# Kernel optimization log

Measured on AMD Instinct MI355X. Metric: run time of the kernel, lower is better.

## Reference

```python
import jax, jax.numpy as jnp
import numpy as np

E = 65536      # num edges
T = 262144     # num triplets
H = 128        # hidden_channels
D = 64         # int_emb_size
C = 8          # basis_emb_size
NR = 6         # num_radial
NS = 7         # num_spherical
NB = 6         # len(bt_list) = num_BT + 1
BT_LIST = (-1, 0, 1, 2, 3, 4)
NBS = 1        # num_before_skip (also used for after-skip list in original code)


def setup_inputs() -> dict:
    key = jax.random.key(0)
    ks = iter(jax.random.split(key, 40))
    s = 0.05
    p = lambda shape: jax.random.normal(next(ks), shape, dtype=jnp.float32) * s
    inp = dict(
        x=jax.random.normal(next(ks), (E, H), dtype=jnp.float32),
        rbf=jax.random.normal(next(ks), (E, NR), dtype=jnp.float32),
        sbf=jax.random.normal(next(ks), (T, NS * NR), dtype=jnp.float32),
        idx_kj=jax.random.randint(next(ks), (T,), 0, E),
        idx_ji=jax.random.randint(next(ks), (T,), 0, E),
        bt=jax.random.randint(next(ks), (E,), 0, 5),
        lambda_d=1,
        alpha=jnp.float32(0.7),
        # per-branch stacked weights (6 branches)
        W_kj=p((NB, H, H)), b_kj=jnp.zeros((NB, H), jnp.float32),
        W_rbf1=p((NB, NR, C)), W_rbf2=p((NB, C, H)),
        W_sbf1=p((NB, NS * NR, C)), W_sbf2=p((NB, C, D)),
        W_down=p((NB, H, D)),
        W_ji=p((H, H)), b_ji=jnp.zeros((H,), jnp.float32),
        W_up=p((D, H)),
        rb1_w=p((NBS, H, H)), rb1_b=jnp.zeros((NBS, H), jnp.float32),
        rb2_w=p((NBS, H, H)), rb2_b=jnp.zeros((NBS, H), jnp.float32),
        W_lin=p((H, H)), b_lin=jnp.zeros((H,), jnp.float32),
        ra1_w=p((NBS, H, H)), ra1_b=jnp.zeros((NBS, H), jnp.float32),
        ra2_w=p((NBS, H, H)), ra2_b=jnp.zeros((NBS, H), jnp.float32),
    )
    return inp


def reference(x, rbf, sbf, idx_kj, idx_ji, bt, lambda_d, alpha,
              W_kj, b_kj, W_rbf1, W_rbf2, W_sbf1, W_sbf2, W_down,
              W_ji, b_ji, W_up, rb1_w, rb1_b, rb2_w, rb2_b,
              W_lin, b_lin, ra1_w, ra1_b, ra2_w, ra2_b):
    act = jax.nn.silu

    x_ji = act(x @ W_ji + b_ji)                                  # [E,H]

    # per-branch edge transforms, vectorized over the 6 branches (axis b)
    tmp = act(jnp.einsum('eh,bhg->beg', x, W_kj) + b_kj[:, None, :])   # [B,E,H]
    rbf_p = jnp.einsum('er,brc->bec', rbf, W_rbf1)                     # [B,E,C]
    rbf_p = jnp.einsum('bec,bcg->beg', rbf_p, W_rbf2)                  # [B,E,H]
    tmp = tmp * rbf_p
    down = act(jnp.einsum('beh,bhd->bed', tmp, W_down))                # [B,E,D]

    sbf_p = jnp.einsum('ts,bsc->btc', sbf, W_sbf1)                     # [B,T,C]
    sbf_p = jnp.einsum('btc,bcd->btd', sbf_p, W_sbf2)                  # [B,T,D]

    spe = down[:, idx_kj, :] * sbf_p                                   # [B,T,D]

    # last branch scattered with weight alpha
    x_kj_tot = alpha * jax.ops.segment_sum(spe[-1], idx_ji, num_segments=E)

    # per band-type masked scatter with weight (1 - alpha)
    bt_trip = bt[idx_kj]                                               # [T]
    for b, btv in enumerate(BT_LIST):
        m = (bt_trip == btv).astype(x.dtype)[:, None]
        x_kj_tot = x_kj_tot + (1.0 - alpha) * jax.ops.segment_sum(
            spe[b] * m, idx_ji, num_segments=E)

    x_kj = act(x_kj_tot @ W_up)                                        # [E,H]
    h = x_ji + x_kj
    for i in range(rb1_w.shape[0]):
        h = h + act(act(h @ rb1_w[i] + rb1_b[i]) @ rb2_w[i] + rb2_b[i])
    h = act(h @ W_lin + b_lin) + x
    for i in range(ra1_w.shape[0]):
        h = h + act(act(h @ ra1_w[i] + ra1_b[i]) @ ra2_w[i] + ra2_b[i])
    return h
```

## Files before the change

kernel.cpp:

```cpp
#include <hip/hip_runtime.h>
#include <hip/hip_bf16.h>
#include <stdint.h>

typedef __bf16 bf16_t;
typedef bf16_t bf16x8 __attribute__((ext_vector_type(8)));
typedef bf16_t bf16x2 __attribute__((ext_vector_type(2)));
typedef float f32x4 __attribute__((ext_vector_type(4)));

#define E_N 65536
#define T_N 262144
#define CAP 16
#define OVF_MAX T_N

__device__ __forceinline__ float silu_f(float v) {
  return v / (1.0f + __expf(-v));
}

__device__ __forceinline__ int permrow(int n) {
  return (n & ~31) | ((n & 1) << 4) | ((n & 30) >> 1);
}

__device__ __forceinline__ uint32_t pack_bf16(float a, float b) {
  union { bf16x2 h; uint32_t u; } u;
  u.h[0] = (bf16_t)a; u.h[1] = (bf16_t)b;
  return u.u;
}

__device__ __forceinline__ void g2l16(const void* g, void* l) {
  __builtin_amdgcn_global_load_lds(
      (const __attribute__((address_space(1))) void*)g,
      (__attribute__((address_space(3))) void*)l, 16, 0, 0);
}

template<int KI, int NTJ>
__device__ __forceinline__ void gemm_tile(const bf16_t* A, const bf16_t* B,
                                          int mb, int nb, int l16, int q,
                                          f32x4 (&acc)[2][NTJ]) {
#pragma unroll
  for (int kt = 0; kt < KI; ++kt) {
    const int sw = ((kt * 4 + q) ^ l16) << 3;
    bf16x8 a0 = *(const bf16x8*)(A + ((mb + l16) << 7) + sw);
    bf16x8 a1 = *(const bf16x8*)(A + ((mb + 16 + l16) << 7) + sw);
#pragma unroll
    for (int tj = 0; tj < NTJ; ++tj) {
      bf16x8 b = *(const bf16x8*)(B + ((nb + tj * 16 + l16) << 7) + sw);
      acc[0][tj] = __builtin_amdgcn_mfma_f32_16x16x32_bf16(a0, b, acc[0][tj], 0, 0, 0);
      acc[1][tj] = __builtin_amdgcn_mfma_f32_16x16x32_bf16(a1, b, acc[1][tj], 0, 0, 0);
    }
  }
}

template<int C4>
__device__ __forceinline__ void stage_x(bf16_t* dst, const float* src, int tid) {
  const float4* g = (const float4*)src;
#pragma unroll
  for (int i = tid; i < 64 * C4; i += 256) {
    const int row = i / C4, c4 = i % C4;
    float4 v = g[i];
    bf16_t t[4] = {(bf16_t)v.x, (bf16_t)v.y, (bf16_t)v.z, (bf16_t)v.w};
    *(uint2*)(dst + (row << 7) + ((((c4 >> 1) ^ (row & 15)) << 3) | ((c4 & 1) << 2))) =
        *(const uint2*)t;
  }
}

__global__ __launch_bounds__(256, 4)
void prep_c8_kernel(
    const float* __restrict__ W_ji, const float* __restrict__ W_kj,
    const float* __restrict__ W_down, const float* __restrict__ W_up,
    const float* __restrict__ rb1, const float* __restrict__ rb2,
    const float* __restrict__ W_lin, const float* __restrict__ ra1,
    const float* __restrict__ ra2, const float* __restrict__ W_rbf1,
    const float* __restrict__ W_rbf2, const float* __restrict__ x,
    char* __restrict__ wm_img, char* __restrict__ wdn_img,
    char* __restrict__ pset, bf16_t* __restrict__ wcb,
    bf16_t* __restrict__ ximg,
    const float* __restrict__ sbf, const int* __restrict__ idx_kj,
    const int* __restrict__ idx_ji, const int* __restrict__ bt,
    const float* __restrict__ Wsbf1,
    float* __restrict__ c8g, uint32_t* __restrict__ meta,
    int* __restrict__ cnt, int* __restrict__ list,
    int* __restrict__ ovf)
{
  __shared__ __align__(16) union {
    bf16_t tile[64 * 128];
    struct {
      float s_sbf[64 * 44];
      float s_W1[2016];
      float s_c8[64 * 16];
      int s_bs[64];
    } c;
  } S;

  const int tid = threadIdx.x;
  const int blk = blockIdx.x;

  if (blk < 4096) {
    const int base = blk * 64;

    for (int i = tid; i < 2016; i += 256) S.c.s_W1[i] = Wsbf1[i];
    if (tid < 64) {
      const int t = base + tid;
      const int kj = idx_kj[t];
      const int ji = idx_ji[t];
      const int bs = bt[kj] + 1;
      S.c.s_bs[tid] = bs;
      meta[t] = (uint32_t)kj | ((uint32_t)bs << 16);
      const int pos = atomicAdd(&cnt[ji], 1);
      if (pos < CAP) {
        list[ji * CAP + pos] = t;
      } else {
        const int o = atomicAdd(&ovf[0], 1);
        if (o < OVF_MAX) { ovf[2 + 2 * o] = t; ovf[2 + 2 * o + 1] = ji; }
      }
    }
    {
      const float2* sg = (const float2*)(sbf + (size_t)base * 42);
      for (int i = tid; i < 64 * 21; i += 256) {
        const int r = i / 21, c2 = i - r * 21;
        const float2 v = sg[i];
        S.c.s_sbf[r * 44 + c2 * 2] = v.x;
        S.c.s_sbf[r * 44 + c2 * 2 + 1] = v.y;
      }
    }
    __syncthreads();

    {
      const int i = tid >> 2;
      const int brr = (tid >> 1) & 1;
      const int cg = tid & 1;
      const int b = brr ? S.c.s_bs[i] : 5;
      const float* w = &S.c.s_W1[b * 336 + cg * 4];
      const float* sb = &S.c.s_sbf[i * 44];
      float a0 = 0.f, a1 = 0.f, a2 = 0.f, a3 = 0.f;
#pragma unroll
      for (int s = 0; s < 42; ++s) {
        const float sv = sb[s];
        const float* ws = w + s * 8;
        a0 += sv * ws[0]; a1 += sv * ws[1]; a2 += sv * ws[2]; a3 += sv * ws[3];
      }
      float* dc = &S.c.s_c8[i * 16 + brr * 8 + cg * 4];
      dc[0] = a0; dc[1] = a1; dc[2] = a2; dc[3] = a3;
    }
    __syncthreads();

    {
      const float4* s4 = (const float4*)S.c.s_c8;
      float4* g4 = (float4*)(c8g + (size_t)base * 16);
      g4[tid] = s4[tid];
    }
    return;
  }

  const int pblk = blk - 4096;
  if (pblk >= 115) {
    const int t = pblk - 115;
    stage_x<32>(S.tile, x + (size_t)t * 8192, tid);
    __syncthreads();
    uint4* dst = (uint4*)(ximg + (size_t)t * 8192);
    const uint4* s = (const uint4*)S.tile;
#pragma unroll
    for (int i = 0; i < 4; ++i) dst[i * 256 + tid] = s[i * 256 + tid];
    return;
  }
  if (pblk >= 112) {
    const int o = (pblk - 112) * 256 + tid;
    if (o < 640) {
      const int b = o >> 7, n = o & 127;
      bf16_t t[8];
#pragma unroll
      for (int r = 0; r < 6; ++r) {
        const float* w1 = W_rbf1 + (b + 1) * 48 + r * 8;
        const float* w2 = W_rbf2 + (b + 1) * 1024 + n;
        float s = 0.f;
#pragma unroll
        for (int c = 0; c < 8; ++c) s += w1[c] * w2[c * 128];
        t[r] = (bf16_t)s;
      }
      t[6] = (bf16_t)0.f; t[7] = (bf16_t)0.f;
      *(uint4*)(wcb + (b * 128 + n) * 8) = *(const uint4*)t;
    }
    return;
  }
  if (pblk >= 108) {
    const int item = (pblk - 108) * 256 + tid;
    const int n = item >> 3, k8 = item & 7;
    bf16_t t[8];
#pragma unroll
    for (int j = 0; j < 8; ++j) t[j] = (bf16_t)W_up[(k8 * 8 + j) * 128 + n];
    const int row = permrow(n);
    *(uint4*)((bf16_t*)pset + (row << 7) + ((k8 ^ (row & 15)) << 3)) = *(const uint4*)t;
    return;
  }
  if (pblk >= 88) {
    const int item = (pblk - 88) * 256 + tid;
    const int m = item >> 10, w = item & 1023;
    const int n = w >> 4, k8 = w & 15;
    const float* src = W_down + (m + 1) * 8192;
    bf16_t* img = (bf16_t*)(wdn_img + m * 16384);
    bf16_t t[8];
#pragma unroll
    for (int j = 0; j < 8; ++j) t[j] = (bf16_t)src[(k8 * 8 + j) * 64 + n];
    const int row = permrow(n);
    *(uint4*)(img + (row << 7) + ((k8 ^ (row & 15)) << 3)) = *(const uint4*)t;
    return;
  }
  const int item = pblk * 256 + tid;
  const int m = item >> 11, w = item & 2047;
  const int n = w >> 4, k8 = w & 15;
  const float* src; char* img;
  if (m == 0)      { src = W_ji;             img = wm_img; }
  else if (m <= 5) { src = W_kj + m * 16384; img = wm_img + m * 32768; }
  else if (m == 6) { src = rb1;   img = pset + 1 * 32768; }
  else if (m == 7) { src = rb2;   img = pset + 2 * 32768; }
  else if (m == 8) { src = W_lin; img = pset + 3 * 32768; }
  else if (m == 9) { src = ra1;   img = pset + 4 * 32768; }
  else             { src = ra2;   img = pset + 5 * 32768; }
  bf16_t t[8];
#pragma unroll
  for (int j = 0; j < 8; ++j) t[j] = (bf16_t)src[(k8 * 8 + j) * 128 + n];
  const int row = permrow(n);
  *(uint4*)((bf16_t*)img + (row << 7) + ((k8 ^ (row & 15)) << 3)) = *(const uint4*)t;
}

__global__ __launch_bounds__(256, 3)
void edge_kernel(const bf16_t* __restrict__ ximg, const float* __restrict__ rbf,
                 const float* __restrict__ b_kj, const float* __restrict__ b_ji,
                 const char* __restrict__ wm_img, const char* __restrict__ wdn_img,
                 const bf16_t* __restrict__ wcb,
                 bf16_t* __restrict__ x_ji_out, bf16_t* __restrict__ down)
{
  __shared__ __align__(16) bf16_t xA[64 * 128];
  __shared__ __align__(16) bf16_t Wb[128 * 128];
  __shared__ __align__(16) bf16_t wcbS[128 * 8];
  __shared__ __align__(16) bf16_t rbfS[64 * 8];
  __shared__ float biasS[128];

  const int tid = threadIdx.x;
  const int lane = tid & 63, wv = tid >> 6;
  const int q = lane >> 4, l16 = lane & 15;
  const int mb = (wv >> 1) * 32, nb = (wv & 1) * 64;
  const int eb = blockIdx.x;
  const int br = eb % 6;
  const int tile = eb / 6;
  const int R = tile * 64;

  {
    const char* xs = (const char*)(ximg + (size_t)tile * 8192);
    char* xd = (char*)xA;
#pragma unroll
    for (int c = 0; c < 4; ++c) {
      const int off = (c * 4 + wv) * 1024 + lane * 16;
      g2l16(xs + off, xd + off);
    }
    const char* wsrc = wm_img + (size_t)br * 32768;
    char* wd = (char*)Wb;
#pragma unroll
    for (int c = 0; c < 8; ++c) {
      const int off = (c * 4 + wv) * 1024 + lane * 16;
      g2l16(wsrc + off, wd + off);
    }
  }
  if (br == 0) {
    if (tid < 128) biasS[tid] = b_ji[tid];
  } else {
    if (tid < 128) biasS[tid] = b_kj[br * 128 + tid];
    if (wv < 2) {
      const char* cs = (const char*)(wcb + (size_t)(br - 1) * 1024);
      const int off = wv * 1024 + lane * 16;
      g2l16(cs + off, (char*)wcbS + off);
    }
    if (tid < 64) {
      const float* rg = rbf + (size_t)(R + tid) * 6;
      bf16_t t[8] = {(bf16_t)rg[0], (bf16_t)rg[1], (bf16_t)rg[2],
                     (bf16_t)rg[3], (bf16_t)rg[4], (bf16_t)rg[5],
                     (bf16_t)0.f, (bf16_t)0.f};
      *(uint4*)(rbfS + tid * 8) = *(const uint4*)t;
    }
  }
  __syncthreads();

  f32x4 acc[2][4] = {};
  gemm_tile<4, 4>(xA, Wb, mb, nb, l16, q, acc);

  if (br == 0) {
#pragma unroll
    for (int ti = 0; ti < 2; ++ti)
#pragma unroll
      for (int r = 0; r < 4; ++r) {
        const int row = mb + ti * 16 + q * 4 + r;
#pragma unroll
        for (int gl = 0; gl < 2; ++gl) {
          const int col0 = nb + gl * 32 + 2 * l16;
          const float2 b2 = *(const float2*)&biasS[col0];
          *(uint32_t*)&x_ji_out[(size_t)(R + row) * 128 + col0] =
              pack_bf16(silu_f(acc[ti][2 * gl][r] + b2.x),
                        silu_f(acc[ti][2 * gl + 1][r] + b2.y));
        }
      }
    return;
  }

  __syncthreads();

  {
    const char* ds = wdn_img + (size_t)(br - 1) * 16384;
    char* dd = (char*)Wb;
#pragma unroll
    for (int c = 0; c < 4; ++c) {
      const int off = (c * 4 + wv) * 1024 + lane * 16;
      g2l16(ds + off, dd + off);
    }
  }

  float wc[2][2][6];
#pragma unroll
  for (int gl = 0; gl < 2; ++gl)
#pragma unroll
    for (int j = 0; j < 2; ++j) {
      const int col = nb + gl * 32 + 2 * l16 + j;
      bf16x8 w8 = *(const bf16x8*)&wcbS[col * 8];
#pragma unroll
      for (int c = 0; c < 6; ++c) wc[gl][j][c] = (float)w8[c];
    }
#pragma unroll
  for (int ti = 0; ti < 2; ++ti)
#pragma unroll
    for (int r = 0; r < 4; ++r) {
      const int row = mb + ti * 16 + q * 4 + r;
      bf16x8 rv8 = *(const bf16x8*)&rbfS[row * 8];
      float rv[6];
#pragma unroll
      for (int c = 0; c < 6; ++c) rv[c] = (float)rv8[c];
#pragma unroll
      for (int gl = 0; gl < 2; ++gl) {
        const int col0 = nb + gl * 32 + 2 * l16;
        const float2 b2 = *(const float2*)&biasS[col0];
        float p0 = 0.f, p1 = 0.f;
#pragma unroll
        for (int c = 0; c < 6; ++c) {
          p0 += rv[c] * wc[gl][0][c];
          p1 += rv[c] * wc[gl][1][c];
        }
        const float v0 = silu_f(acc[ti][2 * gl][r] + b2.x) * p0;
        const float v1 = silu_f(acc[ti][2 * gl + 1][r] + b2.y) * p1;
        *(uint32_t*)&xA[(row << 7) + ((((col0 >> 3) ^ (row & 15)) << 3) | (col0 & 7))] =
            pack_bf16(v0, v1);
      }
    }
  __syncthreads();

  const int nb2 = (wv & 1) * 32;
  f32x4 acc2[2][2] = {};
  gemm_tile<4, 2>(xA, Wb, mb, nb2, l16, q, acc2);
#pragma unroll
  for (int ti = 0; ti < 2; ++ti)
#pragma unroll
    for (int r = 0; r < 4; ++r) {
      const int row = mb + ti * 16 + q * 4 + r;
      const int col0 = nb2 + 2 * l16;
      *(uint32_t*)&down[((size_t)(br - 1) * E_N + R + row) * 64 + col0] =
          pack_bf16(silu_f(acc2[ti][0][r]), silu_f(acc2[ti][1][r]));
    }
}

__global__ __launch_bounds__(256, 8)
void gather_kernel(const int* __restrict__ cnt, const int* __restrict__ list,
                   const uint32_t* __restrict__ meta, const float* __restrict__ c8g,
                   const float* __restrict__ Wsbf2, const bf16_t* __restrict__ down,
                   const float* __restrict__ alpha_p, const int* __restrict__ ovf,
                   float* __restrict__ xkj)
{
  __shared__ float sW2[3072];
  for (int i = threadIdx.x; i < 3072; i += 256) sW2[i] = Wsbf2[i];
  __syncthreads();

  const int e = blockIdx.x * 4 + (threadIdx.x >> 6);
  const int j = threadIdx.x & 63;
  const float alpha = alpha_p[0], oma = 1.f - alpha;
  const float* w5 = &sW2[5 * 512 + j];

  int n = cnt[e];
  if (n > CAP) n = CAP;

  int tk = 0; uint32_t mk = 0;
  if ((j & 15) < n) {
    tk = list[e * CAP + (j & 15)];
    mk = meta[tk];
  }

  float acc = 0.f;
  const int nn = (n + 1) & ~1;
  for (int k0 = 0; k0 < nn; k0 += 2) {
    const int k1 = (k0 + 1 < n) ? k0 + 1 : n - 1;
    const float sc1 = (k0 + 1 < n) ? 1.f : 0.f;
    const int t0 = __builtin_amdgcn_readfirstlane(__shfl(tk, k0, 64));
    const uint32_t m0 = __builtin_amdgcn_readfirstlane(__shfl(mk, k0, 64));
    const int t1 = __builtin_amdgcn_readfirstlane(__shfl(tk, k1, 64));
    const uint32_t m1 = __builtin_amdgcn_readfirstlane(__shfl(mk, k1, 64));
    const int kj0 = m0 & 0xffff, b0 = m0 >> 16;
    const int kj1 = m1 & 0xffff, b1 = m1 >> 16;
    const float g5a = (float)down[((size_t)4 * E_N + kj0) * 64 + j];
    const float gba = (float)down[((size_t)(b0 - 1) * E_N + kj0) * 64 + j];
    const float g5b = (float)down[((size_t)4 * E_N + kj1) * 64 + j];
    const float gbb = (float)down[((size_t)(b1 - 1) * E_N + kj1) * 64 + j];
    const float* cp0 = c8g + (size_t)t0 * 16;
    const float* cp1 = c8g + (size_t)t1 * 16;
    float d5a = 0.f, dba = 0.f, d5b = 0.f, dbb = 0.f;
#pragma unroll
    for (int c = 0; c < 8; ++c) {
      d5a += cp0[c]     * w5[c * 64];
      dba += cp0[8 + c] * sW2[b0 * 512 + c * 64 + j];
      d5b += cp1[c]     * w5[c * 64];
      dbb += cp1[8 + c] * sW2[b1 * 512 + c * 64 + j];
    }
    acc += alpha * g5a * d5a + oma * gba * dba;
    acc += sc1 * (alpha * g5b * d5b + oma * gbb * dbb);
  }

  const int oc = ovf[0];
  for (int k = 0; k < oc; ++k) {
    const int ji = ovf[2 + 2 * k + 1];
    if (ji != e) continue;
    const int t = ovf[2 + 2 * k];
    const uint32_t m = meta[t];
    const int kj = m & 0xffff;
    const int b  = m >> 16;
    const float g5 = (float)down[((size_t)4 * E_N + kj) * 64 + j];
    const float gb = (float)down[((size_t)(b - 1) * E_N + kj) * 64 + j];
    const float* cp = c8g + (size_t)t * 16;
    float d5 = 0.f, db = 0.f;
#pragma unroll
    for (int c = 0; c < 8; ++c) {
      d5 += cp[c]     * w5[c * 64];
      db += cp[8 + c] * sW2[b * 512 + c * 64 + j];
    }
    acc += alpha * g5 * d5 + oma * gb * db;
  }

  xkj[(size_t)e * 64 + j] = acc;
}

__global__ __launch_bounds__(256, 3)
void epi_kernel(const float* __restrict__ x, const bf16_t* __restrict__ x_ji,
                const float* __restrict__ xkj, const char* __restrict__ pset,
                const float* __restrict__ rb1_b, const float* __restrict__ rb2_b,
                const float* __restrict__ lin_b, const float* __restrict__ ra1_b,
                const float* __restrict__ ra2_b,
                float* __restrict__ out)
{
  __shared__ __align__(16) bf16_t buf[64 * 128];
  __shared__ __align__(16) bf16_t Wb[128 * 128];
  __shared__ float biasS[2][128];

  const int tid = threadIdx.x;
  const int lane = tid & 63, wv = tid >> 6;
  const int q = lane >> 4, l16 = lane & 15;
  const int mb = (wv >> 1) * 32, nb = (wv & 1) * 64;
  const int R = blockIdx.x * 64;

#define DMA_W(SLOT) do {                                                         \
    const char* ps_ = pset + (size_t)(SLOT) * 32768;                             \
    char* wd_ = (char*)Wb;                                                       \
    _Pragma("unroll")                                                            \
    for (int c_ = 0; c_ < 8; ++c_) {                                             \
      const int off_ = (c_ * 4 + wv) * 1024 + lane * 16;                         \
      g2l16(ps_ + off_, wd_ + off_);                                             \
    }                                                                            \
  } while (0)

  stage_x<16>(buf, xkj + (size_t)R * 64, tid);
  DMA_W(0);
  __syncthreads();

  f32x4 hreg[2][4];
  {
    f32x4 acc[2][4] = {};
    gemm_tile<2, 4>(buf, Wb, mb, nb, l16, q, acc);
    __syncthreads();
#pragma unroll
    for (int ti = 0; ti < 2; ++ti)
#pragma unroll
      for (int r = 0; r < 4; ++r) {
        const int row = mb + ti * 16 + q * 4 + r;
#pragma unroll
        for (int gl = 0; gl < 2; ++gl) {
          const int col0 = nb + gl * 32 + 2 * l16;
          union { uint32_t u; bf16x2 h; } xj;
          xj.u = *(const uint32_t*)&x_ji[(size_t)(R + row) * 128 + col0];
          const float h0 = (float)xj.h[0] + silu_f(acc[ti][2 * gl][r]);
          const float h1 = (float)xj.h[1] + silu_f(acc[ti][2 * gl + 1][r]);
          hreg[ti][2 * gl][r] = h0;
          hreg[ti][2 * gl + 1][r] = h1;
          *(uint32_t*)&buf[(row << 7) + ((((col0 >> 3) ^ (row & 15)) << 3) | (col0 & 7))] =
              pack_bf16(h0, h1);
        }
      }
    DMA_W(1);
    if (tid < 128) biasS[0][tid] = rb1_b[tid];
    __syncthreads();
  }

#define EPI_STAGE(K, NEXTSLOT, NEXTBIAS, BODY)                                   \
  {                                                                              \
    f32x4 acc[2][4] = {};                                                        \
    gemm_tile<4, 4>(buf, Wb, mb, nb, l16, q, acc);                               \
    __syncthreads();                                                             \
    const float* bs_ = biasS[((K) - 1) & 1];                                     \
    _Pragma("unroll")                                                            \
    for (int ti = 0; ti < 2; ++ti)                                               \
      _Pragma("unroll")                                                          \
      for (int r = 0; r < 4; ++r) {                                              \
        const int row = mb + ti * 16 + q * 4 + r;                                \
        _Pragma("unroll")                                                        \
        for (int gl = 0; gl < 2; ++gl) {                                         \
          const int col0 = nb + gl * 32 + 2 * l16;                               \
          const float2 b2 = *(const float2*)&bs_[col0];                          \
          const float g0 = acc[ti][2 * gl][r] + b2.x;                            \
          const float g1 = acc[ti][2 * gl + 1][r] + b2.y;                        \
          BODY                                                                   \
        }                                                                        \
      }                                                                          \
    if ((K) < 5) {                                                               \
      DMA_W(NEXTSLOT);                                                           \
      if (tid < 128) biasS[(K) & 1][tid] = NEXTBIAS[tid];                        \
      __syncthreads();                                                           \
    }                                                                            \
  }

  EPI_STAGE(1, 2, rb2_b, {
    *(uint32_t*)&buf[(row << 7) + ((((col0 >> 3) ^ (row & 15)) << 3) | (col0 & 7))] =
        pack_bf16(silu_f(g0), silu_f(g1));
  })

  EPI_STAGE(2, 3, lin_b, {
    const float h0 = hreg[ti][2 * gl][r] + silu_f(g0);
    const float h1 = hreg[ti][2 * gl + 1][r] + silu_f(g1);
    hreg[ti][2 * gl][r] = h0; hreg[ti][2 * gl + 1][r] = h1;
    *(uint32_t*)&buf[(row << 7) + ((((col0 >> 3) ^ (row & 15)) << 3) | (col0 & 7))] =
        pack_bf16(h0, h1);
  })

  EPI_STAGE(3, 4, ra1_b, {
    const float2 xv = *(const float2*)&x[(size_t)(R + row) * 128 + col0];
    const float h0 = silu_f(g0) + xv.x;
    const float h1 = silu_f(g1) + xv.y;
    hreg[ti][2 * gl][r] = h0; hreg[ti][2 * gl + 1][r] = h1;
    *(uint32_t*)&buf[(row << 7) + ((((col0 >> 3) ^ (row & 15)) << 3) | (col0 & 7))] =
        pack_bf16(h0, h1);
  })

  EPI_STAGE(4, 5, ra2_b, {
    *(uint32_t*)&buf[(row << 7) + ((((col0 >> 3) ^ (row & 15)) << 3) | (col0 & 7))] =
        pack_bf16(silu_f(g0), silu_f(g1));
  })

  EPI_STAGE(5, 0, ra2_b, {
    float2 o;
    o.x = hreg[ti][2 * gl][r] + silu_f(g0);
    o.y = hreg[ti][2 * gl + 1][r] + silu_f(g1);
    *(float2*)&out[(size_t)(R + row) * 128 + col0] = o;
  })
#undef EPI_STAGE
#undef DMA_W
}

extern "C" void kernel_launch(void* const* d_in, const int* in_sizes, int n_in,
                              void* d_out, int out_size, void* d_ws, size_t ws_size,
                              hipStream_t stream)
{
  (void)in_sizes; (void)n_in; (void)out_size; (void)ws_size;
  const float* x      = (const float*)d_in[0];
  const float* rbf    = (const float*)d_in[1];
  const float* sbf    = (const float*)d_in[2];
  const int*   idx_kj = (const int*)d_in[3];
  const int*   idx_ji = (const int*)d_in[4];
  const int*   bt     = (const int*)d_in[5];
  const float* alpha  = (const float*)d_in[7];
  const float* W_kj   = (const float*)d_in[8];
  const float* b_kj   = (const float*)d_in[9];
  const float* W_rbf1 = (const float*)d_in[10];
  const float* W_rbf2 = (const float*)d_in[11];
  const float* W_sbf1 = (const float*)d_in[12];
  const float* W_sbf2 = (const float*)d_in[13];
  const float* W_down = (const float*)d_in[14];
  const float* W_ji   = (const float*)d_in[15];
  const float* b_ji   = (const float*)d_in[16];
  const float* W_up   = (const float*)d_in[17];
  const float* rb1_w  = (const float*)d_in[18];
  const float* rb1_b  = (const float*)d_in[19];
  const float* rb2_w  = (const float*)d_in[20];
  const float* rb2_b  = (const float*)d_in[21];
  const float* W_lin  = (const float*)d_in[22];
  const float* b_lin  = (const float*)d_in[23];
  const float* ra1_w  = (const float*)d_in[24];
  const float* ra1_b  = (const float*)d_in[25];
  const float* ra2_w  = (const float*)d_in[26];
  const float* ra2_b  = (const float*)d_in[27];

  char* ws = (char*)d_ws;
  bf16_t* down   = (bf16_t*)(ws);
  bf16_t* x_ji   = (bf16_t*)(ws + 41943040);
  bf16_t* ximg   = (bf16_t*)(ws + 58720256);
  float*  xkj    = (float*) (ws + 58720256);
  char*   wm_img = ws + 75497472;
  char*   wdn_img= ws + 75694080;
  char*   pset   = ws + 75776000;
  bf16_t* wcb    = (bf16_t*)(ws + 75972608);
  float*    c8g  = (float*)   (ws + 75982848);
  uint32_t* meta = (uint32_t*)(ws + 92760064);
  int*      list = (int*)     (ws + 93808640);
  int*      cnt  = (int*)     (ws + 98002944);
  int*      ovf  = (int*)     (ws + 98265088);

  hipMemsetAsync(cnt, 0, 262144 + 8, stream);
  prep_c8_kernel<<<5235, 256, 0, stream>>>(W_ji, W_kj, W_down, W_up, rb1_w,
                                           rb2_w, W_lin, ra1_w, ra2_w, W_rbf1,
                                           W_rbf2, x, wm_img, wdn_img, pset,
                                           wcb, ximg, sbf, idx_kj, idx_ji, bt,
                                           W_sbf1, c8g, meta, cnt, list, ovf);
  edge_kernel<<<E_N / 64 * 6, 256, 0, stream>>>(ximg, rbf, b_kj, b_ji, wm_img,
                                                wdn_img, wcb, x_ji, down);
  gather_kernel<<<E_N / 4, 256, 0, stream>>>(cnt, list, meta, c8g, W_sbf2,
                                             down, alpha, ovf, xkj);
  epi_kernel<<<E_N / 64, 256, 0, stream>>>(x, x_ji, xkj, pset,
                                           rb1_b, rb2_b, b_lin, ra1_b, ra2_b,
                                           (float*)d_out);
}
```

Before: 349.8 us.

## Compute band-type branch transforms only for edges of matching band type

Edges are bucketed by band type in the prep kernel using atomic counters, and the edge kernel now computes each branch 1-4 transform only for that branch's bucket of gathered edge rows, writing a single compact down_bt array. Branches 0 (x_ji) and 5 (last branch) are still computed for all edges. This removes the computation and storage of down values that are masked out later, cutting the band-type GEMM work and the down buffer size. In exchange it adds gathered row loads and indirect stores, plus blocks that exit early, and it relies on each edge's down value being read only through its own band type.

```diff
diff --git a/kernel.cpp b/kernel.cpp
--- a/kernel.cpp
+++ b/kernel.cpp
@@ -11,6 +11,7 @@
 #define T_N 262144
 #define CAP 16
 #define OVF_MAX T_N
+#define EINV 0x7fffffff
 
 __device__ __forceinline__ float silu_f(float v) {
   return v / (1.0f + __expf(-v));
@@ -79,7 +80,7 @@
     const float* __restrict__ Wsbf1,
     float* __restrict__ c8g, uint32_t* __restrict__ meta,
     int* __restrict__ cnt, int* __restrict__ list,
-    int* __restrict__ ovf)
+    int* __restrict__ ovf, int* __restrict__ btlist, int* __restrict__ bcnt)
 {
   __shared__ __align__(16) union {
     bf16_t tile[64 * 128];
@@ -150,6 +151,15 @@
     }
     return;
   }
+  if (blk >= 5235) {
+    const int e = (blk - 5235) * 256 + tid;
+    const int bte = bt[e];
+    if (bte < 4) {
+      const int pos = atomicAdd(&bcnt[bte], 1);
+      btlist[bte * E_N + pos] = e;
+    }
+    return;
+  }
 
   const int pblk = blk - 4096;
   if (pblk >= 115) {
@@ -227,7 +237,9 @@
                  const float* __restrict__ b_kj, const float* __restrict__ b_ji,
                  const char* __restrict__ wm_img, const char* __restrict__ wdn_img,
                  const bf16_t* __restrict__ wcb,
-                 bf16_t* __restrict__ x_ji_out, bf16_t* __restrict__ down)
+                 const int* __restrict__ btlist, const int* __restrict__ bcnt,
+                 bf16_t* __restrict__ x_ji_out, bf16_t* __restrict__ down5,
+                 bf16_t* __restrict__ down_bt)
 {
   __shared__ __align__(16) bf16_t xA[64 * 128];
   __shared__ __align__(16) bf16_t Wb[128 * 128];
@@ -239,19 +251,43 @@
   const int lane = tid & 63, wv = tid >> 6;
   const int q = lane >> 4, l16 = lane & 15;
   const int mb = (wv >> 1) * 32, nb = (wv & 1) * 64;
-  const int eb = blockIdx.x;
-  const int br = eb % 6;
-  const int tile = eb / 6;
-  const int R = tile * 64;
-
-  {
-    const char* xs = (const char*)(ximg + (size_t)tile * 8192);
+  const int bid = blockIdx.x;
+
+  int br, R = 0, bkt = 0, cbase = 0, valid = 0;
+  bool bucket = false;
+  if (bid < 1024)      { br = 0; R = bid * 64; }
+  else if (bid < 2048) { br = 5; R = (bid - 1024) * 64; }
+  else {
+    bkt = (bid - 2048) >> 10;
+    cbase = ((bid - 2048) & 1023) * 64;
+    valid = bcnt[bkt];
+    if (cbase >= valid) return;
+    br = bkt + 1;
+    bucket = true;
+  }
+  const int* elist = btlist + bkt * E_N;
+
+  if (!bucket) {
+    const char* xs = (const char*)(ximg + (size_t)(R >> 6) * 8192);
     char* xd = (char*)xA;
 #pragma unroll
     for (int c = 0; c < 4; ++c) {
       const int off = (c * 4 + wv) * 1024 + lane * 16;
       g2l16(xs + off, xd + off);
     }
+  } else {
+    for (int i = tid; i < 1024; i += 256) {
+      const int lr = i >> 4, c = i & 15;
+      const int gidx = cbase + lr;
+      if (gidx < valid) {
+        const int e = elist[gidx];
+        const uint4 v = *(const uint4*)(ximg + ((size_t)(e >> 6) << 13) +
+                                        ((e & 63) << 7) + ((c ^ (e & 15)) << 3));
+        *(uint4*)(xA + (lr << 7) + ((c ^ (lr & 15)) << 3)) = v;
+      }
+    }
+  }
+  {
     const char* wsrc = wm_img + (size_t)br * 32768;
     char* wd = (char*)Wb;
 #pragma unroll
@@ -270,11 +306,16 @@
       g2l16(cs + off, (char*)wcbS + off);
     }
     if (tid < 64) {
-      const float* rg = rbf + (size_t)(R + tid) * 6;
-      bf16_t t[8] = {(bf16_t)rg[0], (bf16_t)rg[1], (bf16_t)rg[2],
-                     (bf16_t)rg[3], (bf16_t)rg[4], (bf16_t)rg[5],
-                     (bf16_t)0.f, (bf16_t)0.f};
-      *(uint4*)(rbfS + tid * 8) = *(const uint4*)t;
+      int e = EINV;
+      if (!bucket) e = R + tid;
+      else if (cbase + tid < valid) e = elist[cbase + tid];
+      if (e != EINV) {
+        const float* rg = rbf + (size_t)e * 6;
+        bf16_t t[8] = {(bf16_t)rg[0], (bf16_t)rg[1], (bf16_t)rg[2],
+                       (bf16_t)rg[3], (bf16_t)rg[4], (bf16_t)rg[5],
+                       (bf16_t)0.f, (bf16_t)0.f};
+        *(uint4*)(rbfS + tid * 8) = *(const uint4*)t;
+      }
     }
   }
   __syncthreads();
@@ -352,13 +393,20 @@
   const int nb2 = (wv & 1) * 32;
   f32x4 acc2[2][2] = {};
   gemm_tile<4, 2>(xA, Wb, mb, nb2, l16, q, acc2);
+  bf16_t* outp = bucket ? down_bt : down5;
 #pragma unroll
   for (int ti = 0; ti < 2; ++ti)
 #pragma unroll
     for (int r = 0; r < 4; ++r) {
       const int row = mb + ti * 16 + q * 4 + r;
+      int e;
+      if (!bucket) e = R + row;
+      else {
+        if (cbase + row >= valid) continue;
+        e = elist[cbase + row];
+      }
       const int col0 = nb2 + 2 * l16;
-      *(uint32_t*)&down[((size_t)(br - 1) * E_N + R + row) * 64 + col0] =
+      *(uint32_t*)&outp[(size_t)e * 64 + col0] =
           pack_bf16(silu_f(acc2[ti][0][r]), silu_f(acc2[ti][1][r]));
     }
 }
@@ -366,7 +414,8 @@
 __global__ __launch_bounds__(256, 8)
 void gather_kernel(const int* __restrict__ cnt, const int* __restrict__ list,
                    const uint32_t* __restrict__ meta, const float* __restrict__ c8g,
-                   const float* __restrict__ Wsbf2, const bf16_t* __restrict__ down,
+                   const float* __restrict__ Wsbf2, const bf16_t* __restrict__ down5,
+                   const bf16_t* __restrict__ down_bt,
                    const float* __restrict__ alpha_p, const int* __restrict__ ovf,
                    float* __restrict__ xkj)
 {
@@ -399,10 +448,12 @@
     const uint32_t m1 = __builtin_amdgcn_readfirstlane(__shfl(mk, k1, 64));
     const int kj0 = m0 & 0xffff, b0 = m0 >> 16;
     const int kj1 = m1 & 0xffff, b1 = m1 >> 16;
-    const float g5a = (float)down[((size_t)4 * E_N + kj0) * 64 + j];
-    const float gba = (float)down[((size_t)(b0 - 1) * E_N + kj0) * 64 + j];
-    const float g5b = (float)down[((size_t)4 * E_N + kj1) * 64 + j];
-    const float gbb = (float)down[((size_t)(b1 - 1) * E_N + kj1) * 64 + j];
+    const bf16_t* pb0 = (b0 == 5) ? down5 : down_bt;
+    const bf16_t* pb1 = (b1 == 5) ? down5 : down_bt;
+    const float g5a = (float)down5[(size_t)kj0 * 64 + j];
+    const float gba = (float)pb0[(size_t)kj0 * 64 + j];
+    const float g5b = (float)down5[(size_t)kj1 * 64 + j];
+    const float gbb = (float)pb1[(size_t)kj1 * 64 + j];
     const float* cp0 = c8g + (size_t)t0 * 16;
     const float* cp1 = c8g + (size_t)t1 * 16;
     float d5a = 0.f, dba = 0.f, d5b = 0.f, dbb = 0.f;
@@ -425,8 +476,9 @@
     const uint32_t m = meta[t];
     const int kj = m & 0xffff;
     const int b  = m >> 16;
-    const float g5 = (float)down[((size_t)4 * E_N + kj) * 64 + j];
-    const float gb = (float)down[((size_t)(b - 1) * E_N + kj) * 64 + j];
+    const bf16_t* pb = (b == 5) ? down5 : down_bt;
+    const float g5 = (float)down5[(size_t)kj * 64 + j];
+    const float gb = (float)pb[(size_t)kj * 64 + j];
     const float* cp = c8g + (size_t)t * 16;
     float d5 = 0.f, db = 0.f;
 #pragma unroll
@@ -598,30 +650,34 @@
   const float* ra2_b  = (const float*)d_in[27];
 
   char* ws = (char*)d_ws;
-  bf16_t* down   = (bf16_t*)(ws);
-  bf16_t* x_ji   = (bf16_t*)(ws + 41943040);
-  bf16_t* ximg   = (bf16_t*)(ws + 58720256);
-  float*  xkj    = (float*) (ws + 58720256);
-  char*   wm_img = ws + 75497472;
-  char*   wdn_img= ws + 75694080;
-  char*   pset   = ws + 75776000;
-  bf16_t* wcb    = (bf16_t*)(ws + 75972608);
-  float*    c8g  = (float*)   (ws + 75982848);
-  uint32_t* meta = (uint32_t*)(ws + 92760064);
-  int*      list = (int*)     (ws + 93808640);
-  int*      cnt  = (int*)     (ws + 98002944);
-  int*      ovf  = (int*)     (ws + 98265088);
-
-  hipMemsetAsync(cnt, 0, 262144 + 8, stream);
-  prep_c8_kernel<<<5235, 256, 0, stream>>>(W_ji, W_kj, W_down, W_up, rb1_w,
+  bf16_t* down5   = (bf16_t*)(ws);
+  bf16_t* down_bt = (bf16_t*)(ws + 8388608);
+  bf16_t* x_ji    = (bf16_t*)(ws + 16777216);
+  bf16_t* ximg    = (bf16_t*)(ws + 33554432);
+  float*  xkj     = (float*) (ws + 50331648);
+  char*   wm_img  = ws + 67108864;
+  char*   wdn_img = ws + 67305472;
+  char*   pset    = ws + 67387392;
+  bf16_t* wcb     = (bf16_t*)(ws + 67584000);
+  float*    c8g   = (float*)   (ws + 67594240);
+  uint32_t* meta  = (uint32_t*)(ws + 84371456);
+  int*      list  = (int*)     (ws + 85420032);
+  int*      btlist= (int*)     (ws + 89614336);
+  int*      cnt   = (int*)     (ws + 90662912);
+  int*      bcnt  = (int*)     (ws + 90925056);
+  int*      ovf   = (int*)     (ws + 90925072);
+
+  hipMemsetAsync(cnt, 0, 262144 + 16 + 8, stream);
+  prep_c8_kernel<<<5491, 256, 0, stream>>>(W_ji, W_kj, W_down, W_up, rb1_w,
                                            rb2_w, W_lin, ra1_w, ra2_w, W_rbf1,
                                            W_rbf2, x, wm_img, wdn_img, pset,
                                            wcb, ximg, sbf, idx_kj, idx_ji, bt,
-                                           W_sbf1, c8g, meta, cnt, list, ovf);
-  edge_kernel<<<E_N / 64 * 6, 256, 0, stream>>>(ximg, rbf, b_kj, b_ji, wm_img,
-                                                wdn_img, wcb, x_ji, down);
+                                           W_sbf1, c8g, meta, cnt, list, ovf,
+                                           btlist, bcnt);
+  edge_kernel<<<6144, 256, 0, stream>>>(ximg, rbf, b_kj, b_ji, wm_img, wdn_img,
+                                        wcb, btlist, bcnt, x_ji, down5, down_bt);
   gather_kernel<<<E_N / 4, 256, 0, stream>>>(cnt, list, meta, c8g, W_sbf2,
-                                             down, alpha, ovf, xkj);
+                                             down5, down_bt, alpha, ovf, xkj);
   epi_kernel<<<E_N / 64, 256, 0, stream>>>(x, x_ji, xkj, pset,
                                            rb1_b, rb2_b, b_lin, ra1_b, ra2_b,
                                            (float*)d_out);
```

Result: slower. 605.5 us (+73.1%).
